# Optimization experiments

Measured on AMD Instinct MI355X. Metric: run time of the kernel, lower is better.

Reference implementation:

```python
import jax, jax.numpy as jnp
import numpy as np

B, C, H, W = 2, 192, 48, 512
EMB, HEADS, DOUT, MAXM, THR, EPS = 64, 2, 192, 64, 0.01, 1e-5
DV = DOUT // HEADS  # per-head value dim (96)


def setup_inputs() -> dict:
    key = jax.random.key(0)
    ks = jax.random.split(key, 16)
    s = 0.02
    inp = {
        "l": jax.random.normal(ks[0], (B, C, H, W), jnp.float32),
        "r": jax.random.normal(ks[1], (B, C, H, W), jnp.float32),
        "ln_l_g": jnp.ones((C,), jnp.float32),
        "ln_l_b": jnp.zeros((C,), jnp.float32),
        "ln_r_g": jnp.ones((C,), jnp.float32),
        "ln_r_b": jnp.zeros((C,), jnp.float32),
    }
    ki = 2
    for p in ("rtl", "ltr"):
        inp[p + "_wq"] = jax.random.normal(ks[ki], (HEADS * EMB, C, 3), jnp.float32) * s; ki += 1
        inp[p + "_bq"] = jnp.zeros((HEADS * EMB,), jnp.float32)
        inp[p + "_wk"] = jax.random.normal(ks[ki], (HEADS * EMB, C, 3), jnp.float32) * s; ki += 1
        inp[p + "_bk"] = jnp.zeros((HEADS * EMB,), jnp.float32)
        inp[p + "_wv"] = jax.random.normal(ks[ki], (DOUT, C, 3), jnp.float32) * s; ki += 1
        inp[p + "_bv"] = jnp.zeros((DOUT,), jnp.float32)
        inp[p + "_wo"] = jax.random.normal(ks[ki], (DOUT, DOUT), jnp.float32) * s; ki += 1
        inp[p + "_bo"] = jnp.zeros((DOUT,), jnp.float32)
    inp["ffl_w"] = jax.random.normal(ks[ki], (DOUT, DOUT), jnp.float32) * s; ki += 1
    inp["ffl_b"] = jnp.zeros((DOUT,), jnp.float32)
    inp["ffr_w"] = jax.random.normal(ks[ki], (DOUT, DOUT), jnp.float32) * s; ki += 1
    inp["ffr_b"] = jnp.zeros((DOUT,), jnp.float32)
    return inp


def _layernorm(x, g, b):
    m = x.mean(-1, keepdims=True)
    v = x.var(-1, keepdims=True)
    return (x - m) / jnp.sqrt(v + EPS) * g + b


def _conv1d(x, w, b):
    # x: [N, Cin, L], w: [Cout, Cin, 3], same padding
    y = jax.lax.conv_general_dilated(x, w, (1,), [(1, 1)], dimension_numbers=("NCH", "OIH", "NCH"))
    return y + b[None, :, None]


def _conv_attn(q_seq, k_seq, v_seq, wq, bq, wk, bk, wv, bv, wo, bo, mask):
    # q_seq/k_seq/v_seq: [N, L, C]; mask: [L, L] bool (True = masked)
    N, L, _ = q_seq.shape
    Q = _conv1d(q_seq.transpose(0, 2, 1), wq, bq).reshape(N, HEADS, EMB, L).transpose(0, 1, 3, 2)  # b h l d
    K = _conv1d(k_seq.transpose(0, 2, 1), wk, bk).reshape(N, HEADS, EMB, L).transpose(0, 1, 3, 2)
    V = _conv1d(v_seq.transpose(0, 2, 1), wv, bv).reshape(N, HEADS, DV, L).transpose(0, 1, 3, 2)
    A = jnp.einsum("bhqd,bhkd->bhqk", Q, K) / np.sqrt(EMB).astype(np.float32)
    A = jnp.where(mask, -jnp.inf, A)
    A = jax.nn.softmax(A, axis=-1)
    A = A * (A > THR)  # valid_mask thresholding after softmax
    O = jnp.einsum("bhqk,bhkd->bhqd", A, V)
    O = O.transpose(0, 2, 1, 3).reshape(N, L, DOUT)
    return jnp.einsum("nld,od->nlo", O, wo) + bo, A


def reference(l, r, ln_l_g, ln_l_b, ln_r_g, ln_r_b,
              rtl_wq, rtl_bq, rtl_wk, rtl_bk, rtl_wv, rtl_bv, rtl_wo, rtl_bo,
              ltr_wq, ltr_bq, ltr_wk, ltr_bk, ltr_wv, ltr_bv, ltr_wo, ltr_bo,
              ffl_w, ffl_b, ffr_w, ffr_b):
    ls = l.transpose(0, 2, 3, 1).reshape(B * H, W, C)  # (b h) w c
    rs = r.transpose(0, 2, 3, 1).reshape(B * H, W, C)
    ln_ = _layernorm(ls, ln_l_g, ln_l_b)
    rn_ = _layernorm(rs, ln_r_g, ln_r_b)
    i = jnp.arange(W)[:, None]
    j = jnp.arange(W)[None, :]
    mask_left = (j < i) | (j - i > MAXM)   # left query i attends keys j in [i, i+MAXM]
    mask_right = (j > i) | (i - j > MAXM)  # right query i attends keys j in [i-MAXM, i]
    l_mha, A_rtl = _conv_attn(ln_, rn_, rs, rtl_wq, rtl_bq, rtl_wk, rtl_bk, rtl_wv, rtl_bv, rtl_wo, rtl_bo, mask_left)
    r_mha, A_ltr = _conv_attn(rn_, ln_, ls, ltr_wq, ltr_bq, ltr_wk, ltr_bk, ltr_wv, ltr_bv, ltr_wo, ltr_bo, mask_right)
    lo = ls + l_mha
    ro = rs + r_mha
    lo = lo + (jnp.einsum("nwc,oc->nwo", lo, ffl_w) + ffl_b)
    ro = ro + (jnp.einsum("nwc,oc->nwo", ro, ffr_w) + ffr_b)
    l_out = lo.reshape(B, H, W, C).transpose(0, 3, 1, 2)
    r_out = ro.reshape(B, H, W, C).transpose(0, 3, 1, 2)
    return (l_out, r_out, A_rtl, A_ltr)
```

## Files before the change

### kernel.cpp

```cpp
#include <hip/hip_runtime.h>
#include <cstddef>
#include <cstdint>

constexpr int kC = 192;
constexpr int kW = 512;
constexpr int kHH = 48;

typedef unsigned short u16;
typedef __attribute__((ext_vector_type(8))) short bf16x8;
typedef __attribute__((ext_vector_type(4))) float f32x4;
typedef __attribute__((ext_vector_type(4))) unsigned short us4;

__device__ inline u16 f2bf(float f) {
  union { float f; uint32_t u; } v; v.f = f;
  uint32_t r = v.u + 0x7FFF + ((v.u >> 16) & 1);
  return (u16)(r >> 16);
}
__device__ inline float bf2f(u16 u) {
  return __uint_as_float(((uint32_t)u) << 16);
}

__global__ void __launch_bounds__(256) ln_kernel(
    const float* __restrict__ xl, const float* __restrict__ xr,
    const float* __restrict__ gl, const float* __restrict__ bl,
    const float* __restrict__ gr, const float* __restrict__ br,
    u16* __restrict__ lnl, u16* __restrict__ lraw,
    u16* __restrict__ lnr, u16* __restrict__ rraw) {
  int n = blockIdx.y;
  int w0 = blockIdx.x * 64;
  int side = blockIdx.z;
  const float* x = side ? xr : xl;
  const float* g = side ? gr : gl;
  const float* b = side ? br : bl;
  u16* lnout = side ? lnr : lnl;
  u16* rawout = side ? rraw : lraw;
  int bb = n / kHH, h = n % kHH;
  __shared__ float tile[64][193];
  __shared__ float red[8][64];
  __shared__ float mean_s[64], rstd_s[64];
  int tid = threadIdx.x;
  int lane = tid & 63, wv = tid >> 6;
  for (int c = wv; c < kC; c += 4)
    tile[lane][c] = x[(((size_t)bb * kC + c) * kHH + h) * kW + w0 + lane];
  __syncthreads();
  {
    int w = tid & 63, part = tid >> 6;
    float s = 0.f, s2 = 0.f;
    const float* row = &tile[w][0];
    for (int c = part * 48; c < part * 48 + 48; ++c) {
      float v = row[c];
      s += v; s2 += v * v;
    }
    red[part][w] = s;
    red[part + 4][w] = s2;
  }
  __syncthreads();
  if (tid < 64) {
    float s = red[0][tid] + red[1][tid] + red[2][tid] + red[3][tid];
    float s2 = red[4][tid] + red[5][tid] + red[6][tid] + red[7][tid];
    float m = s * (1.f / 192.f);
    float var = s2 * (1.f / 192.f) - m * m;
    mean_s[tid] = m;
    rstd_s[tid] = rsqrtf(var + 1e-5f);
  }
  __syncthreads();
  for (int u = tid; u < 64 * 48; u += 256) {
    int w = u / 48, c4 = (u % 48) * 4;
    float mm = mean_s[w], rs = rstd_s[w];
    us4 lp, rp;
#pragma unroll
    for (int j = 0; j < 4; ++j) {
      float raw = tile[w][c4 + j];
      rp[j] = f2bf(raw);
      lp[j] = f2bf((raw - mm) * rs * g[c4 + j] + b[c4 + j]);
    }
    size_t idx = ((size_t)n * kW + w0 + w) * kC + c4;
    *reinterpret_cast<us4*>(&lnout[idx]) = lp;
    *reinterpret_cast<us4*>(&rawout[idx]) = rp;
  }
}

__global__ void wprep_all(
    const float* wq0, const float* wk0, const float* wv0,
    const float* wq1, const float* wk1, const float* wv1,
    const float* bq0, const float* bk0, const float* bv0,
    const float* bq1, const float* bk1, const float* bv1,
    const float* wo0, const float* wo1, const float* fw0, const float* fw1,
    u16* __restrict__ wall, u16* __restrict__ pfw, float* __restrict__ ball) {
  int idx = blockIdx.x * 256 + threadIdx.x;
  if (idx < 516096) {
    int dir = idx / 258048, off = idx % 258048;
    const float* src; int soff;
    if (off < 73728) { src = dir ? wq1 : wq0; soff = off; }
    else if (off < 147456) { src = dir ? wk1 : wk0; soff = off - 73728; }
    else { src = dir ? wv1 : wv0; soff = off - 147456; }
    int o = soff / 576, k = soff % 576, t = k / 192, c = k % 192;
    wall[idx] = f2bf(src[((size_t)o * kC + c) * 3 + t]);
  } else if (idx < 516096 + 147456) {
    int i2 = idx - 516096;
    int mat = i2 / 36864, off = i2 % 36864;
    const float* src = mat == 0 ? wo0 : mat == 1 ? wo1 : mat == 2 ? fw0 : fw1;
    pfw[i2] = f2bf(src[off]);
  } else if (idx < 516096 + 147456 + 896) {
    int bi = idx - 516096 - 147456;
    int dir = bi / 448, boff = bi % 448;
    const float* s; int so;
    if (boff < 128) { s = dir ? bq1 : bq0; so = boff; }
    else if (boff < 256) { s = dir ? bk1 : bk0; so = boff - 128; }
    else { s = dir ? bv1 : bv0; so = boff - 256; }
    ball[bi] = s[so];
  }
}

template <int NF>
__device__ __forceinline__ void conv_core(
    const u16* __restrict__ in, const u16* __restrict__ w2,
    int n, int l0, u16* As, f32x4 (&acc)[4][NF]) {
  int tid = threadIdx.x;
  int wid = tid >> 6, lane = tid & 63;
  int wm = wid >> 1, wn = wid & 1;
  int lr = lane & 15, g = lane >> 4;
  for (int u = tid; u < 130 * 48; u += 256) {
    int row = u / 48, q = u % 48;
    int l = l0 - 1 + row;
    us4 v = {0, 0, 0, 0};
    if (l >= 0 && l < kW)
      v = *reinterpret_cast<const us4*>(in + ((size_t)n * kW + l) * kC + q * 4);
    *reinterpret_cast<us4*>(&As[row * 200 + q * 4]) = v;
  }
  __syncthreads();
  const u16* wbase = w2 + (size_t)(wn * NF * 16 + lr) * 576 + g * 8;
#pragma unroll
  for (int t = 0; t < 3; ++t) {
#pragma unroll
    for (int c0 = 0; c0 < 192; c0 += 64) {
#pragma unroll
      for (int ks = 0; ks < 2; ++ks) {
        bf16x8 a[4], b[NF];
#pragma unroll
        for (int mf = 0; mf < 4; ++mf)
          a[mf] = *reinterpret_cast<const bf16x8*>(
              &As[(wm * 64 + mf * 16 + lr + t) * 200 + c0 + ks * 32 + g * 8]);
#pragma unroll
        for (int nf = 0; nf < NF; ++nf)
          b[nf] = *reinterpret_cast<const bf16x8*>(
              wbase + (size_t)nf * 16 * 576 + t * 192 + c0 + ks * 32);
#pragma unroll
        for (int mf = 0; mf < 4; ++mf)
#pragma unroll
          for (int nf = 0; nf < NF; ++nf)
            acc[mf][nf] = __builtin_amdgcn_mfma_f32_16x16x32_bf16(a[mf], b[nf], acc[mf][nf], 0, 0, 0);
      }
    }
  }
}

__global__ void __launch_bounds__(256) conv_qk(
    const u16* __restrict__ lnl, const u16* __restrict__ lnr,
    const u16* __restrict__ wall, const float* __restrict__ ball,
    u16* __restrict__ Qbf, u16* __restrict__ Kbf) {
  int l0 = blockIdx.x * 128;
  int jid = blockIdx.y;
  int n = blockIdx.z;
  int dir = jid >> 1, which = jid & 1;
  const u16* in = which == 0 ? (dir ? lnr : lnl) : (dir ? lnl : lnr);
  const u16* w2 = wall + (size_t)dir * 258048 + which * 73728;
  const float* bias = ball + dir * 448 + which * 128;

  __shared__ __attribute__((aligned(16))) u16 As[130 * 200];
  f32x4 acc[4][4] = {};
  conv_core<4>(in, w2, n, l0, As, acc);

  int tid = threadIdx.x;
  int wid = tid >> 6, lane = tid & 63;
  int wm = wid >> 1, wn = wid & 1;
  int lr = lane & 15, g = lane >> 4;
  u16* outp = (which == 0 ? Qbf : Kbf) + (size_t)dir * 6291456;
#pragma unroll
  for (int nf = 0; nf < 4; ++nf) {
    int o = wn * 64 + nf * 16 + lr;
    int hh = o >> 6, e = o & 63;
    float bsv = bias[o];
#pragma unroll
    for (int mf = 0; mf < 4; ++mf) {
#pragma unroll
      for (int rg = 0; rg < 4; ++rg) {
        int l = l0 + wm * 64 + mf * 16 + g * 4 + rg;
        outp[((size_t)(n * 2 + hh) * kW + l) * 64 + e] = f2bf(acc[mf][nf][rg] + bsv);
      }
    }
  }
}

__global__ void __launch_bounds__(256) conv_v(
    const u16* __restrict__ lraw, const u16* __restrict__ rraw,
    const u16* __restrict__ wall, const float* __restrict__ ball,
    u16* __restrict__ Vbf) {
  int l0 = blockIdx.x * 128;
  int dir = blockIdx.y;
  int n = blockIdx.z;
  const u16* in = dir ? lraw : rraw;
  const u16* w2 = wall + (size_t)dir * 258048 + 147456;
  const float* bias = ball + dir * 448 + 256;

  __shared__ __attribute__((aligned(16))) u16 As[130 * 200];
  f32x4 acc[4][6] = {};
  conv_core<6>(in, w2, n, l0, As, acc);

  int tid = threadIdx.x;
  int wid = tid >> 6, lane = tid & 63;
  int wm = wid >> 1, wn = wid & 1;
  int lr = lane & 15, g = lane >> 4;
  u16* outp = Vbf + (size_t)dir * 9437184;
#pragma unroll
  for (int nf = 0; nf < 6; ++nf) {
    int e = nf * 16 + lr;
    float bsv = bias[wn * 96 + e];
#pragma unroll
    for (int mf = 0; mf < 4; ++mf) {
      int lb = l0 + wm * 64 + mf * 16 + g * 4;
      us4 p;
#pragma unroll
      for (int rg = 0; rg < 4; ++rg) p[rg] = f2bf(acc[mf][nf][rg] + bsv);
      *reinterpret_cast<us4*>(&outp[((size_t)(n * 2 + wn) * 96 + e) * kW + lb]) = p;
    }
  }
}

__global__ void __launch_bounds__(256) attn_mfma(
    const u16* __restrict__ Qbf, const u16* __restrict__ Kbf,
    const u16* __restrict__ Vbf, float* __restrict__ Abase,
    u16* __restrict__ Obf) {
  int qb = blockIdx.x;
  int nh = blockIdx.y;
  int dir = blockIdx.z;
  int q0 = qb * 64;
  int k_start = dir == 0 ? q0 : (q0 >= 64 ? q0 - 64 : 0);
  int k_end = dir == 0 ? (q0 + 128 <= kW ? q0 + 128 : kW) : q0 + 64;
  int kfr = (k_end - k_start) >> 4;
  const u16* Q = Qbf + ((size_t)dir * 192 + nh) * kW * 64;
  const u16* K = Kbf + ((size_t)dir * 192 + nh) * kW * 64;
  const u16* V = Vbf + ((size_t)dir * 192 + nh) * 96 * kW;
  float* Aout = Abase + (size_t)dir * 50331648 + (size_t)nh * kW * kW;
  u16* Obase = Obf + (size_t)dir * 9437184;

  __shared__ __attribute__((aligned(16))) u16 smem[26880];
  u16* Qs = smem;
  u16* Ks = smem + 4608;
  u16* Ps = smem;
  u16* Vt = smem + 13824;

  int tid = threadIdx.x;
  int wid = tid >> 6, lane = tid & 63;
  int lr = lane & 15, g = lane >> 4;

  for (int u = tid; u < 64 * 16; u += 256) {
    int row = u >> 4, c4 = (u & 15) * 4;
    *reinterpret_cast<us4*>(&Qs[row * 72 + c4]) =
        *reinterpret_cast<const us4*>(&Q[(size_t)(q0 + row) * 64 + c4]);
  }
  for (int u = tid; u < 128 * 16; u += 256) {
    int row = u >> 4, c4 = (u & 15) * 4;
    *reinterpret_cast<us4*>(&Ks[row * 72 + c4]) =
        *reinterpret_cast<const us4*>(&K[(size_t)(k_start + row) * 64 + c4]);
  }
  for (int u = tid; u < 96 * 32; u += 256) {
    int row = u >> 5, c4 = (u & 31) * 4;
    *reinterpret_cast<us4*>(&Vt[row * 136 + c4]) =
        *reinterpret_cast<const us4*>(&V[(size_t)row * kW + k_start + c4]);
  }
  __syncthreads();

  f32x4 sT[8];
#pragma unroll
  for (int kf = 0; kf < 8; ++kf) sT[kf] = f32x4{0.f, 0.f, 0.f, 0.f};
#pragma unroll
  for (int kc = 0; kc < 2; ++kc) {
    bf16x8 bq = *reinterpret_cast<const bf16x8*>(&Qs[(wid * 16 + lr) * 72 + kc * 32 + g * 8]);
#pragma unroll
    for (int kf = 0; kf < 8; ++kf) {
      bf16x8 ak = *reinterpret_cast<const bf16x8*>(&Ks[(kf * 16 + lr) * 72 + kc * 32 + g * 8]);
      sT[kf] = __builtin_amdgcn_mfma_f32_16x16x32_bf16(ak, bq, sT[kf], 0, 0, 0);
    }
  }

  int i = q0 + wid * 16 + lr;
  float mx = -INFINITY;
#pragma unroll
  for (int kf = 0; kf < 8; ++kf) {
#pragma unroll
    for (int r = 0; r < 4; ++r) {
      int jj = k_start + kf * 16 + g * 4 + r;
      bool valid = (jj < k_end) &&
                   (dir == 0 ? (jj >= i && jj - i <= 64) : (jj <= i && i - jj <= 64));
      float v = valid ? sT[kf][r] * 0.125f : -INFINITY;
      sT[kf][r] = v;
      mx = fmaxf(mx, v);
    }
  }
  mx = fmaxf(mx, __shfl_xor(mx, 16));
  mx = fmaxf(mx, __shfl_xor(mx, 32));
  float ssum = 0.f;
#pragma unroll
  for (int kf = 0; kf < 8; ++kf) {
#pragma unroll
    for (int r = 0; r < 4; ++r) {
      float e = __expf(sT[kf][r] - mx);
      sT[kf][r] = e;
      ssum += e;
    }
  }
  ssum += __shfl_xor(ssum, 16);
  ssum += __shfl_xor(ssum, 32);
  float inv = 1.f / ssum;

  __syncthreads();

  {
    float* arow = Aout + (size_t)i * kW + k_start;
#pragma unroll
    for (int kf = 0; kf < 8; ++kf) {
      f32x4 pv;
      us4 pb;
#pragma unroll
      for (int r = 0; r < 4; ++r) {
        float p = sT[kf][r] * inv;
        p = (p > 0.01f) ? p : 0.f;
        pv[r] = p;
        pb[r] = f2bf(p);
      }
      *reinterpret_cast<us4*>(&Ps[(wid * 16 + lr) * 136 + kf * 16 + g * 4]) = pb;
      if (kf < kfr)
        __builtin_nontemporal_store(pv, reinterpret_cast<f32x4*>(arow + kf * 16 + g * 4));
    }
  }
  {
    int row = tid >> 2, t4 = tid & 3;
    f32x4 z4 = {0.f, 0.f, 0.f, 0.f};
    float* arow = Aout + (size_t)(q0 + row) * kW;
    for (int c4 = t4; c4 < (k_start >> 2); c4 += 4)
      __builtin_nontemporal_store(z4, reinterpret_cast<f32x4*>(arow + c4 * 4));
    for (int c4 = (k_end >> 2) + t4; c4 < 128; c4 += 4)
      __builtin_nontemporal_store(z4, reinterpret_cast<f32x4*>(arow + c4 * 4));
  }
  __syncthreads();

  f32x4 oacc[6];
#pragma unroll
  for (int ef = 0; ef < 6; ++ef) oacc[ef] = f32x4{0.f, 0.f, 0.f, 0.f};
#pragma unroll
  for (int kc = 0; kc < 4; ++kc) {
    bf16x8 ap = *reinterpret_cast<const bf16x8*>(&Ps[(wid * 16 + lr) * 136 + kc * 32 + g * 8]);
#pragma unroll
    for (int ef = 0; ef < 6; ++ef) {
      bf16x8 bv = *reinterpret_cast<const bf16x8*>(&Vt[(ef * 16 + lr) * 136 + kc * 32 + g * 8]);
      oacc[ef] = __builtin_amdgcn_mfma_f32_16x16x32_bf16(ap, bv, oacc[ef], 0, 0, 0);
    }
  }
  __syncthreads();
  u16* Os2 = smem;
#pragma unroll
  for (int ef = 0; ef < 6; ++ef) {
    int e = ef * 16 + lr;
#pragma unroll
    for (int r = 0; r < 4; ++r)
      Os2[(wid * 16 + g * 4 + r) * 104 + e] = f2bf(oacc[ef][r]);
  }
  __syncthreads();
  int n_ = nh >> 1, h_ = nh & 1;
  for (int u = tid; u < 64 * 24; u += 256) {
    int q = u / 24, c4 = (u % 24) * 4;
    *reinterpret_cast<us4*>(&Obase[((size_t)n_ * kW + q0 + q) * kC + h_ * 96 + c4]) =
        *reinterpret_cast<const us4*>(&Os2[q * 104 + c4]);
  }
}

__global__ void __launch_bounds__(256) projff_mfma(
    const u16* __restrict__ pfw,
    const float* __restrict__ bo0, const float* __restrict__ bo1,
    const float* __restrict__ fb0, const float* __restrict__ fb1,
    const u16* __restrict__ Obf, const u16* __restrict__ lraw,
    const u16* __restrict__ rraw, float* __restrict__ outbase) {
  int l0 = blockIdx.x * 64;
  int z = blockIdx.y;
  int dir = z / 96, n = z % 96;
  const u16* wo2 = pfw + (dir ? 36864 : 0);
  const u16* fw2 = pfw + 73728 + (dir ? 36864 : 0);
  const float* bo_ = dir ? bo1 : bo0;
  const float* fb_ = dir ? fb1 : fb0;
  const u16* Osrc = Obf + (size_t)dir * 9437184;
  const u16* resbf = dir ? rraw : lraw;
  float* outb = outbase + (size_t)dir * 9437184;
  int bb = n / kHH, h = n % kHH;

  __shared__ __attribute__((aligned(16))) u16 Xs[64 * 200];
  __shared__ __attribute__((aligned(16))) u16 Rs[64 * 200];

  int tid = threadIdx.x;
  int wid = tid >> 6, lane = tid & 63;
  int wm = wid >> 1, wn = wid & 1;
  int lr = lane & 15, g = lane >> 4;

  for (int u = tid; u < 64 * 48; u += 256) {
    int row = u / 48, q = u % 48;
    size_t src = ((size_t)n * kW + l0 + row) * kC + q * 4;
    *reinterpret_cast<us4*>(&Xs[row * 200 + q * 4]) =
        *reinterpret_cast<const us4*>(&Osrc[src]);
    *reinterpret_cast<us4*>(&Rs[row * 200 + q * 4]) =
        *reinterpret_cast<const us4*>(&resbf[src]);
  }
  __syncthreads();

  const u16* wobase = wo2 + (size_t)(wn * 96 + lr) * kC + g * 8;
  const u16* fwbase = fw2 + (size_t)(wn * 96 + lr) * kC + g * 8;

  f32x4 accp[2][6] = {};
#pragma unroll
  for (int c0 = 0; c0 < 192; c0 += 64) {
#pragma unroll
    for (int ks = 0; ks < 2; ++ks) {
      bf16x8 a[2], b[6];
#pragma unroll
      for (int m2 = 0; m2 < 2; ++m2)
        a[m2] = *reinterpret_cast<const bf16x8*>(
            &Xs[(wm * 32 + m2 * 16 + lr) * 200 + c0 + ks * 32 + g * 8]);
#pragma unroll
      for (int nf = 0; nf < 6; ++nf)
        b[nf] = *reinterpret_cast<const bf16x8*>(
            wobase + (size_t)nf * 16 * kC + c0 + ks * 32);
#pragma unroll
      for (int m2 = 0; m2 < 2; ++m2)
#pragma unroll
        for (int nf = 0; nf < 6; ++nf)
          accp[m2][nf] = __builtin_amdgcn_mfma_f32_16x16x32_bf16(a[m2], b[nf], accp[m2][nf], 0, 0, 0);
    }
  }
  __syncthreads();
#pragma unroll
  for (int nf = 0; nf < 6; ++nf) {
    int o = wn * 96 + nf * 16 + lr;
    float bv = bo_[o];
#pragma unroll
    for (int m2 = 0; m2 < 2; ++m2) {
#pragma unroll
      for (int r = 0; r < 4; ++r) {
        int l = wm * 32 + m2 * 16 + g * 4 + r;
        float v = accp[m2][nf][r] + bv + bf2f(Rs[l * 200 + o]);
        accp[m2][nf][r] = v;
        Xs[l * 200 + o] = f2bf(v);
      }
    }
  }
  __syncthreads();

  f32x4 accf[2][6] = {};
#pragma unroll
  for (int c0 = 0; c0 < 192; c0 += 64) {
#pragma unroll
    for (int ks = 0; ks < 2; ++ks) {
      bf16x8 a[2], b[6];
#pragma unroll
      for (int m2 = 0; m2 < 2; ++m2)
        a[m2] = *reinterpret_cast<const bf16x8*>(
            &Xs[(wm * 32 + m2 * 16 + lr) * 200 + c0 + ks * 32 + g * 8]);
#pragma unroll
      for (int nf = 0; nf < 6; ++nf)
        b[nf] = *reinterpret_cast<const bf16x8*>(
            fwbase + (size_t)nf * 16 * kC + c0 + ks * 32);
#pragma unroll
      for (int m2 = 0; m2 < 2; ++m2)
#pragma unroll
        for (int nf = 0; nf < 6; ++nf)
          accf[m2][nf] = __builtin_amdgcn_mfma_f32_16x16x32_bf16(a[m2], b[nf], accf[m2][nf], 0, 0, 0);
    }
  }
#pragma unroll
  for (int nf = 0; nf < 6; ++nf) {
    int o = wn * 96 + nf * 16 + lr;
    float bv = fb_[o];
#pragma unroll
    for (int m2 = 0; m2 < 2; ++m2) {
      f32x4 ov;
#pragma unroll
      for (int r = 0; r < 4; ++r)
        ov[r] = accf[m2][nf][r] + bv + accp[m2][nf][r];
      int l = l0 + wm * 32 + m2 * 16 + g * 4;
      *reinterpret_cast<f32x4*>(&outb[(((size_t)bb * kC + o) * kHH + h) * kW + l]) = ov;
    }
  }
}

extern "C" void kernel_launch(void* const* d_in, const int* in_sizes, int n_in,
                              void* d_out, int out_size, void* d_ws, size_t ws_size,
                              hipStream_t stream) {
  const float* l = (const float*)d_in[0];
  const float* r = (const float*)d_in[1];
  float* out = (float*)d_out;
  float* ws = (float*)d_ws;

  u16* lnl_bf  = (u16*)(ws + 0);
  u16* lnr_bf  = (u16*)(ws + 4718592);
  u16* lraw_bf = (u16*)(ws + 9437184);
  u16* rraw_bf = (u16*)(ws + 14155776);
  u16* wall    = (u16*)(ws + 18874368);
  float* ball  = ws + 19136512;
  u16* Qbf     = (u16*)(ws + 19137536);
  u16* Kbf     = (u16*)(ws + 25428992);
  u16* Vbf     = (u16*)(ws + 31720448);
  u16* Obf     = (u16*)(ws + 41157632);
  u16* pfw     = (u16*)(ws + 50594816);

  ln_kernel<<<dim3(8, 96, 2), 256, 0, stream>>>(
      l, r, (const float*)d_in[2], (const float*)d_in[3],
      (const float*)d_in[4], (const float*)d_in[5],
      lnl_bf, lraw_bf, lnr_bf, rraw_bf);

  wprep_all<<<(516096 + 147456 + 896 + 255) / 256, 256, 0, stream>>>(
      (const float*)d_in[6], (const float*)d_in[8], (const float*)d_in[10],
      (const float*)d_in[14], (const float*)d_in[16], (const float*)d_in[18],
      (const float*)d_in[7], (const float*)d_in[9], (const float*)d_in[11],
      (const float*)d_in[15], (const float*)d_in[17], (const float*)d_in[19],
      (const float*)d_in[12], (const float*)d_in[20],
      (const float*)d_in[22], (const float*)d_in[24],
      wall, pfw, ball);

  conv_qk<<<dim3(4, 4, 96), 256, 0, stream>>>(lnl_bf, lnr_bf, wall, ball, Qbf, Kbf);
  conv_v<<<dim3(4, 2, 96), 256, 0, stream>>>(lraw_bf, rraw_bf, wall, ball, Vbf);

  attn_mfma<<<dim3(8, 192, 2), 256, 0, stream>>>(
      Qbf, Kbf, Vbf, out + (size_t)18874368, Obf);

  projff_mfma<<<dim3(8, 192), 256, 0, stream>>>(
      pfw, (const float*)d_in[13], (const float*)d_in[21],
      (const float*)d_in[23], (const float*)d_in[25],
      Obf, lraw_bf, rraw_bf, out);
}
```

Baseline: 397.7 us.

## Merge prep and conv kernels, use 32x32 MFMA, skip masked attention tiles

```diff
diff --git a/kernel.cpp b/kernel.cpp
--- a/kernel.cpp
+++ b/kernel.cpp
@@ -9,6 +9,7 @@
 typedef unsigned short u16;
 typedef __attribute__((ext_vector_type(8))) short bf16x8;
 typedef __attribute__((ext_vector_type(4))) float f32x4;
+typedef __attribute__((ext_vector_type(16))) float f32x16;
 typedef __attribute__((ext_vector_type(4))) unsigned short us4;
 
 __device__ inline u16 f2bf(float f) {
@@ -20,15 +21,49 @@
   return __uint_as_float(((uint32_t)u) << 16);
 }
 
-__global__ void __launch_bounds__(256) ln_kernel(
+__global__ void __launch_bounds__(256) prep_kernel(
     const float* __restrict__ xl, const float* __restrict__ xr,
     const float* __restrict__ gl, const float* __restrict__ bl,
     const float* __restrict__ gr, const float* __restrict__ br,
     u16* __restrict__ lnl, u16* __restrict__ lraw,
-    u16* __restrict__ lnr, u16* __restrict__ rraw) {
-  int n = blockIdx.y;
-  int w0 = blockIdx.x * 64;
-  int side = blockIdx.z;
+    u16* __restrict__ lnr, u16* __restrict__ rraw,
+    const float* wq0, const float* wk0, const float* wv0,
+    const float* wq1, const float* wk1, const float* wv1,
+    const float* bq0, const float* bk0, const float* bv0,
+    const float* bq1, const float* bk1, const float* bv1,
+    const float* wo0, const float* wo1, const float* fw0, const float* fw1,
+    u16* __restrict__ wall, u16* __restrict__ pfw, float* __restrict__ ball) {
+  int bid = blockIdx.x;
+  int tid = threadIdx.x;
+  if (bid >= 1536) {
+    int idx = (bid - 1536) * 256 + tid;
+    if (idx < 516096) {
+      int dir = idx / 258048, off = idx % 258048;
+      const float* src; int soff;
+      if (off < 73728) { src = dir ? wq1 : wq0; soff = off; }
+      else if (off < 147456) { src = dir ? wk1 : wk0; soff = off - 73728; }
+      else { src = dir ? wv1 : wv0; soff = off - 147456; }
+      int o = soff / 576, k = soff % 576, t = k / 192, c = k % 192;
+      wall[idx] = f2bf(src[((size_t)o * kC + c) * 3 + t]);
+    } else if (idx < 516096 + 147456) {
+      int i2 = idx - 516096;
+      int mat = i2 / 36864, off = i2 % 36864;
+      const float* src = mat == 0 ? wo0 : mat == 1 ? wo1 : mat == 2 ? fw0 : fw1;
+      pfw[i2] = f2bf(src[off]);
+    } else if (idx < 516096 + 147456 + 896) {
+      int bi = idx - 516096 - 147456;
+      int dir = bi / 448, boff = bi % 448;
+      const float* s; int so;
+      if (boff < 128) { s = dir ? bq1 : bq0; so = boff; }
+      else if (boff < 256) { s = dir ? bk1 : bk0; so = boff - 128; }
+      else { s = dir ? bv1 : bv0; so = boff - 256; }
+      ball[bi] = s[so];
+    }
+    return;
+  }
+  int w0 = (bid & 7) * 64;
+  int n = (bid >> 3) % 96;
+  int side = bid / 768;
   const float* x = side ? xr : xl;
   const float* g = side ? gr : gl;
   const float* b = side ? br : bl;
@@ -38,7 +73,6 @@
   __shared__ float tile[64][193];
   __shared__ float red[8][64];
   __shared__ float mean_s[64], rstd_s[64];
-  int tid = threadIdx.x;
   int lane = tid & 63, wv = tid >> 6;
   for (int c = wv; c < kC; c += 4)
     tile[lane][c] = x[(((size_t)bb * kC + c) * kHH + h) * kW + w0 + lane];
@@ -80,46 +114,14 @@
   }
 }
 
-__global__ void wprep_all(
-    const float* wq0, const float* wk0, const float* wv0,
-    const float* wq1, const float* wk1, const float* wv1,
-    const float* bq0, const float* bk0, const float* bv0,
-    const float* bq1, const float* bk1, const float* bv1,
-    const float* wo0, const float* wo1, const float* fw0, const float* fw1,
-    u16* __restrict__ wall, u16* __restrict__ pfw, float* __restrict__ ball) {
-  int idx = blockIdx.x * 256 + threadIdx.x;
-  if (idx < 516096) {
-    int dir = idx / 258048, off = idx % 258048;
-    const float* src; int soff;
-    if (off < 73728) { src = dir ? wq1 : wq0; soff = off; }
-    else if (off < 147456) { src = dir ? wk1 : wk0; soff = off - 73728; }
-    else { src = dir ? wv1 : wv0; soff = off - 147456; }
-    int o = soff / 576, k = soff % 576, t = k / 192, c = k % 192;
-    wall[idx] = f2bf(src[((size_t)o * kC + c) * 3 + t]);
-  } else if (idx < 516096 + 147456) {
-    int i2 = idx - 516096;
-    int mat = i2 / 36864, off = i2 % 36864;
-    const float* src = mat == 0 ? wo0 : mat == 1 ? wo1 : mat == 2 ? fw0 : fw1;
-    pfw[i2] = f2bf(src[off]);
-  } else if (idx < 516096 + 147456 + 896) {
-    int bi = idx - 516096 - 147456;
-    int dir = bi / 448, boff = bi % 448;
-    const float* s; int so;
-    if (boff < 128) { s = dir ? bq1 : bq0; so = boff; }
-    else if (boff < 256) { s = dir ? bk1 : bk0; so = boff - 128; }
-    else { s = dir ? bv1 : bv0; so = boff - 256; }
-    ball[bi] = s[so];
-  }
-}
-
 template <int NF>
-__device__ __forceinline__ void conv_core(
+__device__ __forceinline__ void conv_core32(
     const u16* __restrict__ in, const u16* __restrict__ w2,
-    int n, int l0, u16* As, f32x4 (&acc)[4][NF]) {
+    int n, int l0, u16* As, f32x16 (&acc)[2][NF]) {
   int tid = threadIdx.x;
   int wid = tid >> 6, lane = tid & 63;
   int wm = wid >> 1, wn = wid & 1;
-  int lr = lane & 15, g = lane >> 4;
+  int l31 = lane & 31, g32 = lane >> 5;
   for (int u = tid; u < 130 * 48; u += 256) {
     int row = u / 48, q = u % 48;
     int l = l0 - 1 + row;
@@ -129,100 +131,91 @@
     *reinterpret_cast<us4*>(&As[row * 200 + q * 4]) = v;
   }
   __syncthreads();
-  const u16* wbase = w2 + (size_t)(wn * NF * 16 + lr) * 576 + g * 8;
+  const u16* wrow = w2 + (size_t)(wn * NF * 32 + l31) * 576 + g32 * 8;
+  const u16* arow = As + (size_t)(wm * 64 + l31) * 200 + g32 * 8;
 #pragma unroll
   for (int t = 0; t < 3; ++t) {
 #pragma unroll
     for (int c0 = 0; c0 < 192; c0 += 64) {
 #pragma unroll
-      for (int ks = 0; ks < 2; ++ks) {
-        bf16x8 a[4], b[NF];
-#pragma unroll
-        for (int mf = 0; mf < 4; ++mf)
-          a[mf] = *reinterpret_cast<const bf16x8*>(
-              &As[(wm * 64 + mf * 16 + lr + t) * 200 + c0 + ks * 32 + g * 8]);
+      for (int ks = 0; ks < 4; ++ks) {
+        int ko = c0 + ks * 16;
+        bf16x8 a[2], b[NF];
+#pragma unroll
+        for (int mf = 0; mf < 2; ++mf)
+          a[mf] = *reinterpret_cast<const bf16x8*>(arow + (mf * 32 + t) * 200 + ko);
 #pragma unroll
         for (int nf = 0; nf < NF; ++nf)
-          b[nf] = *reinterpret_cast<const bf16x8*>(
-              wbase + (size_t)nf * 16 * 576 + t * 192 + c0 + ks * 32);
-#pragma unroll
-        for (int mf = 0; mf < 4; ++mf)
+          b[nf] = *reinterpret_cast<const bf16x8*>(wrow + (size_t)nf * 32 * 576 + t * 192 + ko);
+#pragma unroll
+        for (int mf = 0; mf < 2; ++mf)
 #pragma unroll
           for (int nf = 0; nf < NF; ++nf)
-            acc[mf][nf] = __builtin_amdgcn_mfma_f32_16x16x32_bf16(a[mf], b[nf], acc[mf][nf], 0, 0, 0);
-      }
-    }
-  }
-}
-
-__global__ void __launch_bounds__(256) conv_qk(
+            acc[mf][nf] = __builtin_amdgcn_mfma_f32_32x32x16_bf16(a[mf], b[nf], acc[mf][nf], 0, 0, 0);
+      }
+    }
+  }
+}
+
+__global__ void __launch_bounds__(256) conv_all(
     const u16* __restrict__ lnl, const u16* __restrict__ lnr,
+    const u16* __restrict__ lraw, const u16* __restrict__ rraw,
     const u16* __restrict__ wall, const float* __restrict__ ball,
-    u16* __restrict__ Qbf, u16* __restrict__ Kbf) {
+    u16* __restrict__ Qbf, u16* __restrict__ Kbf, u16* __restrict__ Vbf) {
   int l0 = blockIdx.x * 128;
   int jid = blockIdx.y;
   int n = blockIdx.z;
-  int dir = jid >> 1, which = jid & 1;
-  const u16* in = which == 0 ? (dir ? lnr : lnl) : (dir ? lnl : lnr);
-  const u16* w2 = wall + (size_t)dir * 258048 + which * 73728;
-  const float* bias = ball + dir * 448 + which * 128;
-
   __shared__ __attribute__((aligned(16))) u16 As[130 * 200];
-  f32x4 acc[4][4] = {};
-  conv_core<4>(in, w2, n, l0, As, acc);
-
   int tid = threadIdx.x;
   int wid = tid >> 6, lane = tid & 63;
   int wm = wid >> 1, wn = wid & 1;
-  int lr = lane & 15, g = lane >> 4;
-  u16* outp = (which == 0 ? Qbf : Kbf) + (size_t)dir * 6291456;
-#pragma unroll
-  for (int nf = 0; nf < 4; ++nf) {
-    int o = wn * 64 + nf * 16 + lr;
-    int hh = o >> 6, e = o & 63;
-    float bsv = bias[o];
-#pragma unroll
-    for (int mf = 0; mf < 4; ++mf) {
-#pragma unroll
-      for (int rg = 0; rg < 4; ++rg) {
-        int l = l0 + wm * 64 + mf * 16 + g * 4 + rg;
-        outp[((size_t)(n * 2 + hh) * kW + l) * 64 + e] = f2bf(acc[mf][nf][rg] + bsv);
-      }
-    }
-  }
-}
-
-__global__ void __launch_bounds__(256) conv_v(
-    const u16* __restrict__ lraw, const u16* __restrict__ rraw,
-    const u16* __restrict__ wall, const float* __restrict__ ball,
-    u16* __restrict__ Vbf) {
-  int l0 = blockIdx.x * 128;
-  int dir = blockIdx.y;
-  int n = blockIdx.z;
-  const u16* in = dir ? lraw : rraw;
-  const u16* w2 = wall + (size_t)dir * 258048 + 147456;
-  const float* bias = ball + dir * 448 + 256;
-
-  __shared__ __attribute__((aligned(16))) u16 As[130 * 200];
-  f32x4 acc[4][6] = {};
-  conv_core<6>(in, w2, n, l0, As, acc);
-
-  int tid = threadIdx.x;
-  int wid = tid >> 6, lane = tid & 63;
-  int wm = wid >> 1, wn = wid & 1;
-  int lr = lane & 15, g = lane >> 4;
-  u16* outp = Vbf + (size_t)dir * 9437184;
-#pragma unroll
-  for (int nf = 0; nf < 6; ++nf) {
-    int e = nf * 16 + lr;
-    float bsv = bias[wn * 96 + e];
-#pragma unroll
-    for (int mf = 0; mf < 4; ++mf) {
-      int lb = l0 + wm * 64 + mf * 16 + g * 4;
-      us4 p;
-#pragma unroll
-      for (int rg = 0; rg < 4; ++rg) p[rg] = f2bf(acc[mf][nf][rg] + bsv);
-      *reinterpret_cast<us4*>(&outp[((size_t)(n * 2 + wn) * 96 + e) * kW + lb]) = p;
+  int l31 = lane & 31, g32 = lane >> 5;
+
+  if (jid < 4) {
+    int dir = jid >> 1, which = jid & 1;
+    const u16* in = which == 0 ? (dir ? lnr : lnl) : (dir ? lnl : lnr);
+    const u16* w2 = wall + (size_t)dir * 258048 + which * 73728;
+    const float* bias = ball + dir * 448 + which * 128;
+    f32x16 acc[2][2] = {};
+    conv_core32<2>(in, w2, n, l0, As, acc);
+    u16* outp = (which == 0 ? Qbf : Kbf) + (size_t)dir * 6291456;
+#pragma unroll
+    for (int nf = 0; nf < 2; ++nf) {
+      int o = wn * 64 + nf * 32 + l31;
+      int hh = o >> 6, e = o & 63;
+      float bsv = bias[o];
+#pragma unroll
+      for (int mf = 0; mf < 2; ++mf) {
+#pragma unroll
+        for (int reg = 0; reg < 16; ++reg) {
+          int l = l0 + wm * 64 + mf * 32 + (reg & 3) + 8 * (reg >> 2) + 4 * g32;
+          outp[((size_t)(n * 2 + hh) * kW + l) * 64 + e] = f2bf(acc[mf][nf][reg] + bsv);
+        }
+      }
+    }
+  } else {
+    int dir = jid - 4;
+    const u16* in = dir ? lraw : rraw;
+    const u16* w2 = wall + (size_t)dir * 258048 + 147456;
+    const float* bias = ball + dir * 448 + 256;
+    f32x16 acc[2][3] = {};
+    conv_core32<3>(in, w2, n, l0, As, acc);
+    u16* outp = Vbf + (size_t)dir * 9437184;
+#pragma unroll
+    for (int nf = 0; nf < 3; ++nf) {
+      int e = nf * 32 + l31;
+      float bsv = bias[wn * 96 + e];
+#pragma unroll
+      for (int mf = 0; mf < 2; ++mf) {
+#pragma unroll
+        for (int r4 = 0; r4 < 4; ++r4) {
+          int lb = l0 + wm * 64 + mf * 32 + 8 * r4 + 4 * g32;
+          us4 p;
+#pragma unroll
+          for (int j = 0; j < 4; ++j) p[j] = f2bf(acc[mf][nf][4 * r4 + j] + bsv);
+          *reinterpret_cast<us4*>(&outp[((size_t)(n * 2 + wn) * 96 + e) * kW + lb]) = p;
+        }
+      }
     }
   }
 }
@@ -271,16 +264,23 @@
   }
   __syncthreads();
 
+  int lo_k = q0 + wid * 16 - (dir == 0 ? 0 : 64) - k_start;
+  int hi_k = q0 + wid * 16 + 15 + (dir == 0 ? 64 : 0) - k_start;
+
   f32x4 sT[8];
 #pragma unroll
   for (int kf = 0; kf < 8; ++kf) sT[kf] = f32x4{0.f, 0.f, 0.f, 0.f};
-#pragma unroll
-  for (int kc = 0; kc < 2; ++kc) {
-    bf16x8 bq = *reinterpret_cast<const bf16x8*>(&Qs[(wid * 16 + lr) * 72 + kc * 32 + g * 8]);
+  {
+    bf16x8 bq0 = *reinterpret_cast<const bf16x8*>(&Qs[(wid * 16 + lr) * 72 + g * 8]);
+    bf16x8 bq1 = *reinterpret_cast<const bf16x8*>(&Qs[(wid * 16 + lr) * 72 + 32 + g * 8]);
 #pragma unroll
     for (int kf = 0; kf < 8; ++kf) {
-      bf16x8 ak = *reinterpret_cast<const bf16x8*>(&Ks[(kf * 16 + lr) * 72 + kc * 32 + g * 8]);
-      sT[kf] = __builtin_amdgcn_mfma_f32_16x16x32_bf16(ak, bq, sT[kf], 0, 0, 0);
+      if (kf * 16 + 15 >= lo_k && kf * 16 <= hi_k) {
+        bf16x8 ak0 = *reinterpret_cast<const bf16x8*>(&Ks[(kf * 16 + lr) * 72 + g * 8]);
+        sT[kf] = __builtin_amdgcn_mfma_f32_16x16x32_bf16(ak0, bq0, sT[kf], 0, 0, 0);
+        bf16x8 ak1 = *reinterpret_cast<const bf16x8*>(&Ks[(kf * 16 + lr) * 72 + 32 + g * 8]);
+        sT[kf] = __builtin_amdgcn_mfma_f32_16x16x32_bf16(ak1, bq1, sT[kf], 0, 0, 0);
+      }
     }
   }
 
@@ -350,11 +350,13 @@
   for (int ef = 0; ef < 6; ++ef) oacc[ef] = f32x4{0.f, 0.f, 0.f, 0.f};
 #pragma unroll
   for (int kc = 0; kc < 4; ++kc) {
-    bf16x8 ap = *reinterpret_cast<const bf16x8*>(&Ps[(wid * 16 + lr) * 136 + kc * 32 + g * 8]);
-#pragma unroll
-    for (int ef = 0; ef < 6; ++ef) {
-      bf16x8 bv = *reinterpret_cast<const bf16x8*>(&Vt[(ef * 16 + lr) * 136 + kc * 32 + g * 8]);
-      oacc[ef] = __builtin_amdgcn_mfma_f32_16x16x32_bf16(ap, bv, oacc[ef], 0, 0, 0);
+    if (kc * 32 + 31 >= lo_k && kc * 32 <= hi_k) {
+      bf16x8 ap = *reinterpret_cast<const bf16x8*>(&Ps[(wid * 16 + lr) * 136 + kc * 32 + g * 8]);
+#pragma unroll
+      for (int ef = 0; ef < 6; ++ef) {
+        bf16x8 bv = *reinterpret_cast<const bf16x8*>(&Vt[(ef * 16 + lr) * 136 + kc * 32 + g * 8]);
+        oacc[ef] = __builtin_amdgcn_mfma_f32_16x16x32_bf16(ap, bv, oacc[ef], 0, 0, 0);
+      }
     }
   }
   __syncthreads();
@@ -510,12 +512,12 @@
   u16* Obf     = (u16*)(ws + 41157632);
   u16* pfw     = (u16*)(ws + 50594816);
 
-  ln_kernel<<<dim3(8, 96, 2), 256, 0, stream>>>(
+  int wp_items = 516096 + 147456 + 896;
+  int wp_blocks = (wp_items + 255) / 256;
+  prep_kernel<<<1536 + wp_blocks, 256, 0, stream>>>(
       l, r, (const float*)d_in[2], (const float*)d_in[3],
       (const float*)d_in[4], (const float*)d_in[5],
-      lnl_bf, lraw_bf, lnr_bf, rraw_bf);
-
-  wprep_all<<<(516096 + 147456 + 896 + 255) / 256, 256, 0, stream>>>(
+      lnl_bf, lraw_bf, lnr_bf, rraw_bf,
       (const float*)d_in[6], (const float*)d_in[8], (const float*)d_in[10],
       (const float*)d_in[14], (const float*)d_in[16], (const float*)d_in[18],
       (const float*)d_in[7], (const float*)d_in[9], (const float*)d_in[11],
@@ -524,8 +526,8 @@
       (const float*)d_in[22], (const float*)d_in[24],
       wall, pfw, ball);
 
-  conv_qk<<<dim3(4, 4, 96), 256, 0, stream>>>(lnl_bf, lnr_bf, wall, ball, Qbf, Kbf);
-  conv_v<<<dim3(4, 2, 96), 256, 0, stream>>>(lraw_bf, rraw_bf, wall, ball, Vbf);
+  conv_all<<<dim3(4, 6, 96), 256, 0, stream>>>(
+      lnl_bf, lnr_bf, lraw_bf, rraw_bf, wall, ball, Qbf, Kbf, Vbf);
 
   attn_mfma<<<dim3(8, 192, 2), 256, 0, stream>>>(
       Qbf, Kbf, Vbf, out + (size_t)18874368, Obf);
```

Result: slower. 407.1 us (+2.4%).
